# Kernel tuning notes

Hardware: AMD Instinct MI355X
Metric: run time of the kernel (lower is better)

## Reference

```python
import jax, jax.numpy as jnp
import numpy as np

L = 7  # window size (odd)
A = 0.1
B_COEF = 0.9


def mex_hat(d):
    grid = (np.mgrid[:d, :d] - d // 2) * 1.0
    eucl = (grid ** 2).sum(0) ** 0.5
    eucl /= d
    return eucl * np.exp(-eucl)


def setup_inputs() -> dict:
    key = jax.random.key(0)
    x = jax.random.normal(key, (16, 1, 512, 512), dtype=jnp.float32)
    kernel = jnp.asarray(mex_hat(L).reshape(-1), dtype=jnp.float32)  # [49], row-major like unfold
    return {"x": x, "kernel": kernel}


def reference(x, kernel):
    # x: [B,1,H,W], kernel: [L*L]
    # Extract zero-padded LxL patches, matching F.unfold(padding=L//2) ordering
    # (C=1, kernel positions row-major). patches: [B, L*L, H, W]
    patches = jax.lax.conv_general_dilated_patches(
        x, (L, L), (1, 1), 'SAME')
    average_term = jnp.exp(-patches.mean(axis=1, keepdims=True))  # [B,1,H,W]
    differential_term = jnp.sum(
        kernel[None, :, None, None] * jax.nn.relu(patches - x),
        axis=1, keepdims=True)  # [B,1,H,W]
    suppression = A * average_term + B_COEF * differential_term
    norm = jnp.sqrt(jnp.sum(suppression ** 2))
    suppression = suppression / norm
    mask = jnp.where(x > suppression, jnp.ones_like(x), jnp.zeros_like(x))
    return mask, average_term, differential_term
```

## Files before the change

kernel.cpp:

```cpp
#include <hip/hip_runtime.h>
#include <math.h>

#define HW 512
#define NB 16
#define TX 32
#define TY 32
#define LDSW 40
#define LDSH 38
#define N_PIX (NB * HW * HW)
#define NBLK (16 * 16 * NB)

using f32x4 = __attribute__((ext_vector_type(4))) float;

__device__ __forceinline__ float sgpr_f(float v) {
    return __uint_as_float(__builtin_amdgcn_readfirstlane(__float_as_uint(v)));
}

__global__ __launch_bounds__(64, 4) void li_phase1(
    const float* __restrict__ x, const float* __restrict__ kw,
    float* __restrict__ out_ratio, float* __restrict__ out_avg,
    float* __restrict__ out_dif, float* __restrict__ partials)
{
    __shared__ float tile[LDSH * LDSW];

    const int tid = threadIdx.x;
    const int bx = blockIdx.x, by = blockIdx.y, b = blockIdx.z;
    const int x0 = bx * TX, y0 = by * TY;
    const float* xb = x + (size_t)b * (HW * HW);

    float w[49];
    float W = 0.f;
#pragma unroll
    for (int i = 0; i < 49; i++) { w[i] = sgpr_f(kw[i]); W += w[i]; }

    for (int idx = tid; idx < LDSH * (LDSW / 4); idx += 64) {
        int r = idx / (LDSW / 4);
        int c4 = idx - r * (LDSW / 4);
        int gy = y0 - 3 + r;
        int gx = x0 - 4 + c4 * 4;
        float4 v = make_float4(0.f, 0.f, 0.f, 0.f);
        if ((unsigned)gy < HW && (unsigned)gx < HW)
            v = *(const float4*)(xb + gy * HW + gx);
        *(float4*)&tile[r * LDSW + c4 * 4] = v;
    }
    __syncthreads();

    const int cx = tid & 7;
    const int cy = tid >> 3;
    const int colw = 4 * cx;
    const int row0 = 4 * cy;

    float cen[16];
#pragma unroll
    for (int p = 0; p < 4; p++) {
        float4 c4v = *(const float4*)&tile[(row0 + 3 + p) * LDSW + colw + 4];
        cen[p*4+0] = c4v.x; cen[p*4+1] = c4v.y; cen[p*4+2] = c4v.z; cen[p*4+3] = c4v.w;
    }

    float dif[16], bsum[16];
#pragma unroll
    for (int k = 0; k < 16; k++) { dif[k] = 0.f; bsum[k] = 0.f; }

#pragma unroll
    for (int r = 0; r < 10; r++) {
        const float* base = &tile[(row0 + r) * LDSW + colw];
        float4 q0 = *(const float4*)base;
        float4 q1 = *(const float4*)(base + 4);
        float4 q2 = *(const float4*)(base + 8);
        float v[12] = {q0.x, q0.y, q0.z, q0.w,
                       q1.x, q1.y, q1.z, q1.w,
                       q2.x, q2.y, q2.z, q2.w};

        float s0 = ((v[1] + v[2]) + (v[3] + v[4])) + ((v[5] + v[6]) + v[7]);
        float s1 = s0 + (v[8]  - v[1]);
        float s2 = s1 + (v[9]  - v[2]);
        float s3 = s2 + (v[10] - v[3]);

#pragma unroll
        for (int p = 0; p < 4; p++) {
            const int di = r - p;
            if (di < 0 || di >= 7) continue;
            bsum[p*4+0] += s0; bsum[p*4+1] += s1;
            bsum[p*4+2] += s2; bsum[p*4+3] += s3;
#pragma unroll
            for (int dj = 0; dj < 7; dj++) {
                if (di == 3 && dj == 3) continue;
                const float wv = w[di*7+dj];
#pragma unroll
                for (int j = 0; j < 4; j++)
                    dif[p*4+j] = fmaf(wv, fmaxf(v[1+j+dj], cen[p*4+j]), dif[p*4+j]);
            }
        }
    }

    const size_t gbase = (size_t)b * (HW * HW) + (size_t)(y0 + row0) * HW + x0 + colw;
    float ss = 0.f;
#pragma unroll
    for (int p = 0; p < 4; p++) {
        float av[4], dv[4], rv[4];
#pragma unroll
        for (int j = 0; j < 4; j++) {
            const int k = p*4+j;
            av[j] = __expf(-bsum[k] * (1.0f / 49.0f));
            dv[j] = fmaf(-W, cen[k], dif[k]);
            const float spv = 0.1f * av[j] + 0.9f * dv[j];
            rv[j] = cen[k] * __builtin_amdgcn_rcpf(spv);
            ss = fmaf(spv, spv, ss);
        }
        const size_t gi = gbase + (size_t)p * HW;
        *(f32x4*)(out_avg + gi)   = (f32x4){av[0], av[1], av[2], av[3]};
        *(f32x4*)(out_dif + gi)   = (f32x4){dv[0], dv[1], dv[2], dv[3]};
        *(f32x4*)(out_ratio + gi) = (f32x4){rv[0], rv[1], rv[2], rv[3]};
    }

#pragma unroll
    for (int off = 32; off > 0; off >>= 1)
        ss += __shfl_down(ss, off, 64);
    if (tid == 0)
        partials[bx + 16 * (by + 16 * b)] = ss;
}

__global__ __launch_bounds__(256) void li_phase2(
    const float* __restrict__ partials, float* __restrict__ io)
{
    __shared__ float wsum[4];
    __shared__ float s_inv;
    const int tid = threadIdx.x;

    float s = 0.f;
#pragma unroll
    for (int i = 0; i < NBLK / 256; i++)
        s += partials[tid + i * 256];
#pragma unroll
    for (int off = 32; off > 0; off >>= 1)
        s += __shfl_down(s, off, 64);
    if ((tid & 63) == 0) wsum[tid >> 6] = s;
    __syncthreads();
    if (tid == 0)
        s_inv = 1.0f / sqrtf((wsum[0] + wsum[1]) + (wsum[2] + wsum[3]));
    __syncthreads();

    const float inv = s_inv;
    const int base = blockIdx.x * 4096 + tid * 4;
#pragma unroll
    for (int k = 0; k < 4; k++) {
        const int i = base + k * 1024;
        float4 r = *(const float4*)(io + i);
        float4 m;
        m.x = (r.x > inv) ? 1.f : 0.f;
        m.y = (r.y > inv) ? 1.f : 0.f;
        m.z = (r.z > inv) ? 1.f : 0.f;
        m.w = (r.w > inv) ? 1.f : 0.f;
        *(float4*)(io + i) = m;
    }
}

extern "C" void kernel_launch(void* const* d_in, const int* in_sizes, int n_in,
                              void* d_out, int out_size, void* d_ws, size_t ws_size,
                              hipStream_t stream) {
    const float* x  = (const float*)d_in[0];
    const float* kw = (const float*)d_in[1];
    float* out   = (float*)d_out;
    float* ratio = out;
    float* avg   = out + N_PIX;
    float* dif   = out + 2 * (size_t)N_PIX;
    float* ws    = (float*)d_ws;

    dim3 g(HW / TX, HW / TY, NB);
    li_phase1<<<g, 64, 0, stream>>>(x, kw, ratio, avg, dif, ws);
    li_phase2<<<N_PIX / 4096, 256, 0, stream>>>(ws, ratio);
}
```

Before: 113.1 us.

## Shrink phase-1 tiles to 16x16 with one pixel row per thread

Phase 1 now uses 16x16 output tiles with a 22x24 LDS halo, and each thread computes one row of 4 pixels instead of a 4x4 block. This drops the vertical register reuse across rows, so each thread needs far fewer registers, and the launch-bounds occupancy hint rises from 4 to 6. The grid becomes four times larger and the partial-sum count grows to match. In exchange, halo overhead per tile is much higher and each output now needs more LDS reads, since the 10-row sliding reuse is gone.

Result: no change. 111.5 us (-1.4%).

```diff
diff --git a/kernel.cpp b/kernel.cpp
--- a/kernel.cpp
+++ b/kernel.cpp
@@ -3,12 +3,12 @@
 
 #define HW 512
 #define NB 16
-#define TX 32
-#define TY 32
-#define LDSW 40
-#define LDSH 38
+#define TX 16
+#define TY 16
+#define LDSW 24
+#define LDSH 22
 #define N_PIX (NB * HW * HW)
-#define NBLK (16 * 16 * NB)
+#define NBLK (32 * 32 * NB)
 
 using f32x4 = __attribute__((ext_vector_type(4))) float;
 
@@ -16,7 +16,7 @@
     return __uint_as_float(__builtin_amdgcn_readfirstlane(__float_as_uint(v)));
 }
 
-__global__ __launch_bounds__(64, 4) void li_phase1(
+__global__ __launch_bounds__(64, 6) void li_phase1(
     const float* __restrict__ x, const float* __restrict__ kw,
     float* __restrict__ out_ratio, float* __restrict__ out_avg,
     float* __restrict__ out_dif, float* __restrict__ partials)
@@ -33,37 +33,38 @@
 #pragma unroll
     for (int i = 0; i < 49; i++) { w[i] = sgpr_f(kw[i]); W += w[i]; }
 
-    for (int idx = tid; idx < LDSH * (LDSW / 4); idx += 64) {
-        int r = idx / (LDSW / 4);
-        int c4 = idx - r * (LDSW / 4);
-        int gy = y0 - 3 + r;
-        int gx = x0 - 4 + c4 * 4;
-        float4 v = make_float4(0.f, 0.f, 0.f, 0.f);
-        if ((unsigned)gy < HW && (unsigned)gx < HW)
-            v = *(const float4*)(xb + gy * HW + gx);
-        *(float4*)&tile[r * LDSW + c4 * 4] = v;
+#pragma unroll
+    for (int k = 0; k < 3; k++) {
+        const int idx = tid + k * 64;
+        if (idx < LDSH * (LDSW / 4)) {
+            const int r  = idx / (LDSW / 4);
+            const int c4 = idx - r * (LDSW / 4);
+            const int gy = y0 - 3 + r;
+            const int gx = x0 - 4 + c4 * 4;
+            float4 v = make_float4(0.f, 0.f, 0.f, 0.f);
+            if ((unsigned)gy < HW && (unsigned)gx <= (unsigned)(HW - 4))
+                v = *(const float4*)(xb + gy * HW + gx);
+            *(float4*)&tile[r * LDSW + c4 * 4] = v;
+        }
     }
     __syncthreads();
 
-    const int cx = tid & 7;
-    const int cy = tid >> 3;
+    const int cx = tid & 3;
+    const int cy = tid >> 2;
     const int colw = 4 * cx;
-    const int row0 = 4 * cy;
 
-    float cen[16];
-#pragma unroll
-    for (int p = 0; p < 4; p++) {
-        float4 c4v = *(const float4*)&tile[(row0 + 3 + p) * LDSW + colw + 4];
-        cen[p*4+0] = c4v.x; cen[p*4+1] = c4v.y; cen[p*4+2] = c4v.z; cen[p*4+3] = c4v.w;
+    float cen[4];
+    {
+        float4 c4v = *(const float4*)&tile[(cy + 3) * LDSW + colw + 4];
+        cen[0] = c4v.x; cen[1] = c4v.y; cen[2] = c4v.z; cen[3] = c4v.w;
     }
 
-    float dif[16], bsum[16];
-#pragma unroll
-    for (int k = 0; k < 16; k++) { dif[k] = 0.f; bsum[k] = 0.f; }
+    float dif[4]  = {0.f, 0.f, 0.f, 0.f};
+    float bsum[4] = {0.f, 0.f, 0.f, 0.f};
 
 #pragma unroll
-    for (int r = 0; r < 10; r++) {
-        const float* base = &tile[(row0 + r) * LDSW + colw];
+    for (int di = 0; di < 7; di++) {
+        const float* base = &tile[(cy + di) * LDSW + colw];
         float4 q0 = *(const float4*)base;
         float4 q1 = *(const float4*)(base + 4);
         float4 q2 = *(const float4*)(base + 8);
@@ -75,49 +76,38 @@
         float s1 = s0 + (v[8]  - v[1]);
         float s2 = s1 + (v[9]  - v[2]);
         float s3 = s2 + (v[10] - v[3]);
+        bsum[0] += s0; bsum[1] += s1; bsum[2] += s2; bsum[3] += s3;
 
 #pragma unroll
-        for (int p = 0; p < 4; p++) {
-            const int di = r - p;
-            if (di < 0 || di >= 7) continue;
-            bsum[p*4+0] += s0; bsum[p*4+1] += s1;
-            bsum[p*4+2] += s2; bsum[p*4+3] += s3;
+        for (int dj = 0; dj < 7; dj++) {
+            if (di == 3 && dj == 3) continue;
+            const float wv = w[di * 7 + dj];
 #pragma unroll
-            for (int dj = 0; dj < 7; dj++) {
-                if (di == 3 && dj == 3) continue;
-                const float wv = w[di*7+dj];
-#pragma unroll
-                for (int j = 0; j < 4; j++)
-                    dif[p*4+j] = fmaf(wv, fmaxf(v[1+j+dj], cen[p*4+j]), dif[p*4+j]);
-            }
+            for (int j = 0; j < 4; j++)
+                dif[j] = fmaf(wv, fmaxf(v[1 + j + dj], cen[j]), dif[j]);
         }
     }
 
-    const size_t gbase = (size_t)b * (HW * HW) + (size_t)(y0 + row0) * HW + x0 + colw;
+    const size_t gi = (size_t)b * (HW * HW) + (size_t)(y0 + cy) * HW + x0 + colw;
+    float av[4], dv[4], rv[4];
     float ss = 0.f;
 #pragma unroll
-    for (int p = 0; p < 4; p++) {
-        float av[4], dv[4], rv[4];
-#pragma unroll
-        for (int j = 0; j < 4; j++) {
-            const int k = p*4+j;
-            av[j] = __expf(-bsum[k] * (1.0f / 49.0f));
-            dv[j] = fmaf(-W, cen[k], dif[k]);
-            const float spv = 0.1f * av[j] + 0.9f * dv[j];
-            rv[j] = cen[k] * __builtin_amdgcn_rcpf(spv);
-            ss = fmaf(spv, spv, ss);
-        }
-        const size_t gi = gbase + (size_t)p * HW;
-        *(f32x4*)(out_avg + gi)   = (f32x4){av[0], av[1], av[2], av[3]};
-        *(f32x4*)(out_dif + gi)   = (f32x4){dv[0], dv[1], dv[2], dv[3]};
-        *(f32x4*)(out_ratio + gi) = (f32x4){rv[0], rv[1], rv[2], rv[3]};
+    for (int j = 0; j < 4; j++) {
+        av[j] = __expf(-bsum[j] * (1.0f / 49.0f));
+        dv[j] = fmaf(-W, cen[j], dif[j]);
+        const float spv = 0.1f * av[j] + 0.9f * dv[j];
+        rv[j] = cen[j] * __builtin_amdgcn_rcpf(spv);
+        ss = fmaf(spv, spv, ss);
     }
+    *(f32x4*)(out_avg + gi)   = (f32x4){av[0], av[1], av[2], av[3]};
+    *(f32x4*)(out_dif + gi)   = (f32x4){dv[0], dv[1], dv[2], dv[3]};
+    *(f32x4*)(out_ratio + gi) = (f32x4){rv[0], rv[1], rv[2], rv[3]};
 
 #pragma unroll
     for (int off = 32; off > 0; off >>= 1)
         ss += __shfl_down(ss, off, 64);
     if (tid == 0)
-        partials[bx + 16 * (by + 16 * b)] = ss;
+        partials[bx + 32 * (by + 32 * b)] = ss;
 }
 
 __global__ __launch_bounds__(256) void li_phase2(
```
